# Optimization experiments

Hardware: AMD Instinct MI355X
Metric: run time of the kernel (lower is better)

## Reference

```python
import jax, jax.numpy as jnp
import numpy as np

N, E = 4096, 4096          # nodes, hyperedges
IN_DIM, OUT_DIM, EDGE_DIM = 256, 256, 64
HEADS, DEG, CARD = 8, 8, 8  # node degree, edge cardinality (regular hypergraph)


def setup_inputs() -> dict:
    key = jax.random.key(0)
    ks = jax.random.split(key, 6)
    # regular hypergraph: DEG rounds, each a permutation of nodes chunked into
    # blocks of CARD -> every node in exactly DEG edges, every edge has CARD
    # distinct nodes. E = DEG * N / CARD.
    rng = np.random.default_rng(0)
    node_of_edge = np.concatenate(
        [rng.permutation(N).reshape(-1, CARD) for _ in range(DEG)], axis=0)  # [E, CARD]
    inc = np.zeros((E, N), dtype=np.float32)
    inc[np.arange(E)[:, None], node_of_edge] = 1.0
    s = 0.05
    return {
        "x": jax.random.normal(ks[0], (N, IN_DIM), jnp.float32),
        "incidence": jnp.asarray(inc),
        "edge_attr": jax.random.normal(ks[1], (E, EDGE_DIM), jnp.float32),
        "W_lin": jax.random.normal(ks[2], (IN_DIM, OUT_DIM), jnp.float32) * s,
        "W_edge": jax.random.normal(ks[3], (EDGE_DIM, OUT_DIM), jnp.float32) * s,
        "in_proj_w": jax.random.normal(ks[4], (3 * OUT_DIM, OUT_DIM), jnp.float32) * s,
        "in_proj_b": jnp.zeros((3 * OUT_DIM,), jnp.float32),
        "out_proj_w": jax.random.normal(ks[5], (OUT_DIM, OUT_DIM), jnp.float32) * s,
        "out_proj_b": jnp.zeros((OUT_DIM,), jnp.float32),
        "deg": DEG,
        "card": CARD,
    }


def reference(x, incidence, edge_attr, W_lin, W_edge,
              in_proj_w, in_proj_b, out_proj_w, out_proj_b, deg, card):
    n = x.shape[0]
    Wh = x @ W_lin          # [N, D]
    We = edge_attr @ W_edge  # [E, D]
    Dm = Wh.shape[1]
    H = HEADS
    dh = Dm // H
    # recover regular structure from the binary incidence matrix.
    # (attention is permutation-invariant over the pair set, so the order of
    #  indices returned by top_k vs torch.nonzero does not matter)
    _, edge_of_node = jax.lax.top_k(incidence.T, deg)   # [N, deg]
    _, node_of_edge = jax.lax.top_k(incidence, card)    # [E, card]
    pair_e = edge_of_node[:, :, None]                   # [N, deg, 1]
    pair_u = node_of_edge[edge_of_node]                 # [N, deg, card]
    L = deg * card
    Ksrc = (Wh[pair_u] + We[pair_e]).reshape(n, L, Dm)  # key source per pair
    Vsrc = Wh[pair_u].reshape(n, L, Dm)                 # value source per pair
    # torch nn.MultiheadAttention in/out projections
    Wq, Wk, Wv = jnp.split(in_proj_w, 3, axis=0)
    bq, bk, bv = jnp.split(in_proj_b, 3)
    q = (Wh @ Wq.T + bq).reshape(n, H, dh)              # q_len = 1 per node
    k = (Ksrc @ Wk.T + bk).reshape(n, L, H, dh)
    v = (Vsrc @ Wv.T + bv).reshape(n, L, H, dh)
    scale = 1.0 / jnp.sqrt(jnp.asarray(dh, q.dtype))
    scores = jnp.einsum('nhd,nlhd->nhl', q, k) * scale  # [N, H, L]
    attn = jax.nn.softmax(scores, axis=-1)
    ctx = jnp.einsum('nhl,nlhd->nhd', attn, v).reshape(n, Dm)
    out = ctx @ out_proj_w.T + out_proj_b
    return jax.nn.relu(out)
```

## Files before the change

kernel.cpp:

```cpp
#include <hip/hip_runtime.h>
#include <hip/hip_bf16.h>

#define NN    4096
#define EE    4096
#define DM    256
#define EDIM  64
#define HH    8
#define DHd   32
#define LL    64

typedef short  s16x8 __attribute__((ext_vector_type(8)));
typedef unsigned short u16x8 __attribute__((ext_vector_type(8)));
typedef float  f32x4 __attribute__((ext_vector_type(4)));

__device__ __forceinline__ float b2f(unsigned short u) {
  return __uint_as_float(((unsigned int)u) << 16);
}
__device__ __forceinline__ unsigned short f2b_bits(float f) {
  unsigned int u = __float_as_uint(f);
  u = (u + 0x7FFFu + ((u >> 16) & 1u)) >> 16;
  return (unsigned short)u;
}

__global__ __launch_bounds__(256) void f2b_all(
    const float* __restrict__ x, const float* __restrict__ ea,
    const float* __restrict__ ipw, const float* __restrict__ wlin,
    const float* __restrict__ wedge, const float* __restrict__ wout,
    unsigned short* __restrict__ xb, unsigned short* __restrict__ eab,
    unsigned short* __restrict__ ipwb, unsigned short* __restrict__ wlinb,
    unsigned short* __restrict__ wedgeb, unsigned short* __restrict__ woutb,
    int* __restrict__ cnt) {
  int i = blockIdx.x * 256 + threadIdx.x;
  if (i < 8192) cnt[i] = 0;
  const float* src; unsigned short* dst; int j = i;
  if (j < 262144)       { src = x;     dst = xb; }
  else { j -= 262144;
  if (j < 65536)        { src = ea;    dst = eab; }
  else { j -= 65536;
  if (j < 49152)        { src = ipw;   dst = ipwb; }
  else { j -= 49152;
  if (j < 16384)        { src = wlin;  dst = wlinb; }
  else { j -= 16384;
  if (j < 4096)         { src = wedge; dst = wedgeb; }
  else { j -= 4096;
  if (j >= 16384) return;
                          src = wout;  dst = woutb; }}}}}
  float4 v = ((const float4*)src)[j];
  ushort4 o;
  o.x = f2b_bits(v.x); o.y = f2b_bits(v.y); o.z = f2b_bits(v.z); o.w = f2b_bits(v.w);
  ((ushort4*)dst)[j] = o;
}

#define MODE_PLAIN 0
#define MODE_PROJ  1
#define MODE_OUT   2

__device__ __forceinline__ void gemm_tile(
    const unsigned short* __restrict__ A, const unsigned short* __restrict__ B,
    int i0, int j0, int N, int K, int mode,
    float* __restrict__ out_f, unsigned short* __restrict__ out_b,
    unsigned short* __restrict__ out_b2, const float* __restrict__ bias,
    short* As, short* Bs) {
  const int tid  = threadIdx.x;
  const int wid  = tid >> 6, lane = tid & 63;
  const int wr   = (wid >> 1) * 32, wc = (wid & 1) * 32;
  const int srow = tid >> 2, schunk = (tid & 3) * 8;
  const int fr   = lane & 15, fk = (lane >> 4) * 8;

  f32x4 acc[2][2];
#pragma unroll
  for (int a = 0; a < 2; ++a)
#pragma unroll
    for (int b = 0; b < 2; ++b) acc[a][b] = (f32x4){0.f, 0.f, 0.f, 0.f};

  for (int kk = 0; kk < K; kk += 32) {
    *(s16x8*)&As[srow * 40 + schunk] = *(const s16x8*)&A[(size_t)(i0 + srow) * K + kk + schunk];
    *(s16x8*)&Bs[srow * 40 + schunk] = *(const s16x8*)&B[(size_t)(j0 + srow) * K + kk + schunk];
    __syncthreads();
    s16x8 af0 = *(const s16x8*)&As[(wr + fr) * 40 + fk];
    s16x8 af1 = *(const s16x8*)&As[(wr + 16 + fr) * 40 + fk];
    s16x8 bf0 = *(const s16x8*)&Bs[(wc + fr) * 40 + fk];
    s16x8 bf1 = *(const s16x8*)&Bs[(wc + 16 + fr) * 40 + fk];
    acc[0][0] = __builtin_amdgcn_mfma_f32_16x16x32_bf16(af0, bf0, acc[0][0], 0, 0, 0);
    acc[0][1] = __builtin_amdgcn_mfma_f32_16x16x32_bf16(af0, bf1, acc[0][1], 0, 0, 0);
    acc[1][0] = __builtin_amdgcn_mfma_f32_16x16x32_bf16(af1, bf0, acc[1][0], 0, 0, 0);
    acc[1][1] = __builtin_amdgcn_mfma_f32_16x16x32_bf16(af1, bf1, acc[1][1], 0, 0, 0);
    __syncthreads();
  }

  const int ecol = lane & 15, erow0 = (lane >> 4) * 4;
#pragma unroll
  for (int mi = 0; mi < 2; ++mi)
#pragma unroll
    for (int ni = 0; ni < 2; ++ni) {
#pragma unroll
      for (int v = 0; v < 4; ++v) {
        int i = i0 + wr + mi * 16 + erow0 + v;
        int j = j0 + wc + ni * 16 + ecol;
        float val = acc[mi][ni][v];
        if (mode == MODE_PLAIN) {
          out_b[(size_t)i * N + j] = f2b_bits(val);
        } else if (mode == MODE_PROJ) {
          if (j < 256)      out_f[(size_t)i * 256 + j]          = val + bias[j];
          else if (j < 512) out_b[(size_t)i * 256 + (j - 256)]  = f2b_bits(val);
          else              out_b2[(size_t)i * 256 + (j - 512)] = f2b_bits(val + bias[j]);
        } else {
          float r = val + bias[j];
          out_f[(size_t)i * N + j] = r > 0.f ? r : 0.f;
        }
      }
    }
}

__global__ __launch_bounds__(256) void adj_fusew(
    const float* __restrict__ inc,
    int* __restrict__ cnt_e, int* __restrict__ cnt_n,
    int* __restrict__ noe, int* __restrict__ eon,
    const unsigned short* __restrict__ ipw_bf, const unsigned short* __restrict__ wlin_bf,
    const unsigned short* __restrict__ wedg_bf,
    unsigned short* __restrict__ F, unsigned short* __restrict__ G) {
  __shared__ short As[64 * 40] __attribute__((aligned(16)));
  __shared__ short Bs[64 * 40] __attribute__((aligned(16)));
  const int bid = blockIdx.x;
  if (bid < 16384) {
    int t = bid * 256 + threadIdx.x;
    float4 v = ((const float4*)inc)[t];
    int flat = t * 4;
    int e  = flat >> 12;
    int u0 = flat & 4095;
    float vals[4] = {v.x, v.y, v.z, v.w};
#pragma unroll
    for (int j = 0; j < 4; ++j) {
      if (vals[j] != 0.0f) {
        int u  = u0 + j;
        int pe = atomicAdd(&cnt_e[e], 1);
        noe[e * 8 + pe] = u;
        int pn = atomicAdd(&cnt_n[u], 1);
        eon[u * 8 + pn] = e;
      }
    }
    return;
  }
  int fb = bid - 16384;
  if (fb < 48) {
    gemm_tile(ipw_bf, wlin_bf, (fb >> 2) * 64, (fb & 3) * 64, 256, 256,
              MODE_PLAIN, nullptr, F, nullptr, nullptr, As, Bs);
  } else {
    gemm_tile(ipw_bf + 256 * 256, wedg_bf, (fb - 48) * 64, 0, 64, 256,
              MODE_PLAIN, nullptr, G, nullptr, nullptr, As, Bs);
  }
}

__global__ __launch_bounds__(256) void proj_ke(
    const unsigned short* __restrict__ x_bf, const unsigned short* __restrict__ F,
    const unsigned short* __restrict__ ea_bf, const unsigned short* __restrict__ G,
    float* __restrict__ q, unsigned short* __restrict__ Kn, unsigned short* __restrict__ Vn,
    unsigned short* __restrict__ Ke, const float* __restrict__ ipb) {
  __shared__ short As[64 * 40] __attribute__((aligned(16)));
  __shared__ short Bs[64 * 40] __attribute__((aligned(16)));
  const int bid = blockIdx.x;
  if (bid < 768) {
    gemm_tile(x_bf, F, (bid & 63) * 64, (bid >> 6) * 64, 768, 256,
              MODE_PROJ, q, Kn, Vn, ipb, As, Bs);
  } else {
    int r = bid - 768;
    gemm_tile(ea_bf, G, (r & 63) * 64, (r >> 6) * 64, 256, 64,
              MODE_PLAIN, nullptr, Ke, nullptr, nullptr, As, Bs);
  }
}

__global__ __launch_bounds__(256) void gemm_out(
    const unsigned short* __restrict__ ctx, const unsigned short* __restrict__ wout_bf,
    float* __restrict__ out, const float* __restrict__ bias) {
  __shared__ short As[64 * 40] __attribute__((aligned(16)));
  __shared__ short Bs[64 * 40] __attribute__((aligned(16)));
  gemm_tile(ctx, wout_bf, blockIdx.x * 64, blockIdx.y * 64, 256, 256,
            MODE_OUT, out, nullptr, nullptr, bias, As, Bs);
}

__global__ __launch_bounds__(512) void attn_kernel(
    const float* __restrict__ q, const unsigned short* __restrict__ Kn,
    const unsigned short* __restrict__ Vn, const unsigned short* __restrict__ Ke,
    const int* __restrict__ eon, const int* __restrict__ noe,
    unsigned short* __restrict__ ctx) {
  const int n = blockIdx.x;
  __shared__ int   e_s[8];
  __shared__ int   u_s[64];
  __shared__ float q_s[256];
  __shared__ float qke_s[64];
  const int tid = threadIdx.x;
  if (tid < 8) e_s[tid] = eon[n * 8 + tid];
  if (tid >= 256 && tid < 320)
    ((float4*)q_s)[tid - 256] = ((const float4*)(q + (size_t)n * 256))[tid - 256];
  __syncthreads();
  if (tid < 64) {
    u_s[tid] = noe[e_s[tid >> 3] * 8 + (tid & 7)];
  } else if (tid < 128) {
    const int h = (tid - 64) >> 3, e = tid & 7;
    const u16x8* ep = (const u16x8*)(Ke + (size_t)e_s[e] * 256 + h * 32);
    float s = 0.f;
#pragma unroll
    for (int c = 0; c < 4; ++c) {
      u16x8 ev = ep[c];
#pragma unroll
      for (int j = 0; j < 8; ++j) s += q_s[h * 32 + c * 8 + j] * b2f(ev[j]);
    }
    qke_s[(h << 3) | e] = s;
  }
  __syncthreads();

  const int h = tid >> 6, lane = tid & 63;
  const int dchunk = lane >> 4, rg = lane & 15;

  u16x8 vstage[4];
#pragma unroll
  for (int i = 0; i < 4; ++i)
    vstage[i] = *(const u16x8*)(Vn + (size_t)u_s[rg * 4 + i] * 256 + h * 32 + dchunk * 8);

  const int u = u_s[lane];
  const u16x8* kp = (const u16x8*)(Kn + ((size_t)u * 256 + h * 32));
  float s = 0.f;
#pragma unroll
  for (int c = 0; c < 4; ++c) {
    u16x8 kv = kp[c];
#pragma unroll
    for (int j = 0; j < 8; ++j) s += q_s[h * 32 + c * 8 + j] * b2f(kv[j]);
  }
  s = (s + qke_s[(h << 3) | (lane >> 3)]) * 0.17677669529663687f;

  float m = s;
#pragma unroll
  for (int off = 32; off >= 1; off >>= 1) m = fmaxf(m, __shfl_xor(m, off));
  float p = __expf(s - m);
  float sum = p;
#pragma unroll
  for (int off = 32; off >= 1; off >>= 1) sum += __shfl_xor(sum, off);
  const float a = p / sum;

  float acc[8];
#pragma unroll
  for (int j = 0; j < 8; ++j) acc[j] = 0.f;
#pragma unroll
  for (int i = 0; i < 4; ++i) {
    float pi = __shfl(a, rg * 4 + i, 64);
#pragma unroll
    for (int j = 0; j < 8; ++j) acc[j] += pi * b2f(vstage[i][j]);
  }
#pragma unroll
  for (int off = 1; off < 16; off <<= 1)
#pragma unroll
    for (int j = 0; j < 8; ++j) acc[j] += __shfl_xor(acc[j], off, 64);

  if (rg == 0) {
    u16x8 o;
#pragma unroll
    for (int j = 0; j < 8; ++j) o[j] = f2b_bits(acc[j]);
    *(u16x8*)(ctx + (size_t)n * 256 + h * 32 + dchunk * 8) = o;
  }
}

#define OFF_Q      ((size_t)0)
#define OFF_KN     ((size_t)4194304)
#define OFF_VN     ((size_t)6291456)
#define OFF_KE     ((size_t)8388608)
#define OFF_CTX    ((size_t)10485760)
#define OFF_XBF    ((size_t)12582912)
#define OFF_EABF   ((size_t)14680064)
#define OFF_WOUTBF ((size_t)15204352)
#define OFF_IPWBF  ((size_t)15335424)
#define OFF_WLINBF ((size_t)15728640)
#define OFF_WEDGBF ((size_t)15859712)
#define OFF_F      ((size_t)15892480)
#define OFF_G      ((size_t)16285696)
#define OFF_CNTE   ((size_t)16318464)
#define OFF_CNTN   ((size_t)16334848)
#define OFF_NOE    ((size_t)16351232)
#define OFF_EON    ((size_t)16482304)

extern "C" void kernel_launch(void* const* d_in, const int* in_sizes, int n_in,
                              void* d_out, int out_size, void* d_ws, size_t ws_size,
                              hipStream_t stream) {
  const float* x     = (const float*)d_in[0];
  const float* inc   = (const float*)d_in[1];
  const float* ea    = (const float*)d_in[2];
  const float* wlin  = (const float*)d_in[3];
  const float* wedge = (const float*)d_in[4];
  const float* ipw   = (const float*)d_in[5];
  const float* ipb   = (const float*)d_in[6];
  const float* wout  = (const float*)d_in[7];
  const float* outb  = (const float*)d_in[8];

  char* ws = (char*)d_ws;
  float*          q       = (float*)(ws + OFF_Q);
  unsigned short* Kn      = (unsigned short*)(ws + OFF_KN);
  unsigned short* Vn      = (unsigned short*)(ws + OFF_VN);
  unsigned short* Ke      = (unsigned short*)(ws + OFF_KE);
  unsigned short* ctx     = (unsigned short*)(ws + OFF_CTX);
  unsigned short* x_bf    = (unsigned short*)(ws + OFF_XBF);
  unsigned short* ea_bf   = (unsigned short*)(ws + OFF_EABF);
  unsigned short* wout_bf = (unsigned short*)(ws + OFF_WOUTBF);
  unsigned short* ipw_bf  = (unsigned short*)(ws + OFF_IPWBF);
  unsigned short* wlin_bf = (unsigned short*)(ws + OFF_WLINBF);
  unsigned short* wedg_bf = (unsigned short*)(ws + OFF_WEDGBF);
  unsigned short* F       = (unsigned short*)(ws + OFF_F);
  unsigned short* G       = (unsigned short*)(ws + OFF_G);
  int*            cnt_e   = (int*)(ws + OFF_CNTE);
  int*            cnt_n   = (int*)(ws + OFF_CNTN);
  int*            noe     = (int*)(ws + OFF_NOE);
  int*            eon     = (int*)(ws + OFF_EON);

  f2b_all<<<1616, 256, 0, stream>>>(x, ea, ipw, wlin, wedge, wout,
                                    x_bf, ea_bf, ipw_bf, wlin_bf, wedg_bf, wout_bf,
                                    cnt_e);
  adj_fusew<<<16436, 256, 0, stream>>>(inc, cnt_e, cnt_n, noe, eon,
                                       ipw_bf, wlin_bf, wedg_bf, F, G);
  proj_ke<<<1024, 256, 0, stream>>>(x_bf, F, ea_bf, G, q, Kn, Vn, Ke, ipb);
  attn_kernel<<<4096, 512, 0, stream>>>(q, Kn, Vn, Ke, eon, noe, ctx);
  gemm_out<<<dim3(64, 4), 256, 0, stream>>>(ctx, wout_bf, (float*)d_out, outb);
}
```

Measured before the change: 83.51 us.

## Fuse conversion into adjacency kernel, precompute pair indices, restructure attention per wave

The separate fp32-to-bf16 conversion kernel is removed. Activation conversion is merged into the adjacency-building kernel, weight-product GEMMs now read fp32 weights directly, and the counter zeroing moves to a memset. Q is stored as bf16 with the softmax scale folded into the projection epilogue. Pair node indices are precomputed in the projection kernel, and attention now runs one wave per (node, head) with no shared memory or block syncs. The aim is fewer launches, less traffic and less synchronisation, at the cost of extra bf16 rounding of q and a memset launch.

```diff
diff --git a/kernel.cpp b/kernel.cpp
--- a/kernel.cpp
+++ b/kernel.cpp
@@ -13,6 +13,8 @@
 typedef unsigned short u16x8 __attribute__((ext_vector_type(8)));
 typedef float  f32x4 __attribute__((ext_vector_type(4)));
 
+#define SCALE 0.17677669529663687f
+
 __device__ __forceinline__ float b2f(unsigned short u) {
   return __uint_as_float(((unsigned int)u) << 16);
 }
@@ -22,38 +24,21 @@
   return (unsigned short)u;
 }
 
-__global__ __launch_bounds__(256) void f2b_all(
-    const float* __restrict__ x, const float* __restrict__ ea,
-    const float* __restrict__ ipw, const float* __restrict__ wlin,
-    const float* __restrict__ wedge, const float* __restrict__ wout,
-    unsigned short* __restrict__ xb, unsigned short* __restrict__ eab,
-    unsigned short* __restrict__ ipwb, unsigned short* __restrict__ wlinb,
-    unsigned short* __restrict__ wedgeb, unsigned short* __restrict__ woutb,
-    int* __restrict__ cnt) {
-  int i = blockIdx.x * 256 + threadIdx.x;
-  if (i < 8192) cnt[i] = 0;
-  const float* src; unsigned short* dst; int j = i;
-  if (j < 262144)       { src = x;     dst = xb; }
-  else { j -= 262144;
-  if (j < 65536)        { src = ea;    dst = eab; }
-  else { j -= 65536;
-  if (j < 49152)        { src = ipw;   dst = ipwb; }
-  else { j -= 49152;
-  if (j < 16384)        { src = wlin;  dst = wlinb; }
-  else { j -= 16384;
-  if (j < 4096)         { src = wedge; dst = wedgeb; }
-  else { j -= 4096;
-  if (j >= 16384) return;
-                          src = wout;  dst = woutb; }}}}}
-  float4 v = ((const float4*)src)[j];
-  ushort4 o;
-  o.x = f2b_bits(v.x); o.y = f2b_bits(v.y); o.z = f2b_bits(v.z); o.w = f2b_bits(v.w);
-  ((ushort4*)dst)[j] = o;
-}
-
 #define MODE_PLAIN 0
 #define MODE_PROJ  1
 #define MODE_OUT   2
+
+__device__ __forceinline__ void gemm_mfma_body(
+    short* As, short* Bs, f32x4 acc[2][2], int wr, int wc, int fr, int fk) {
+  s16x8 af0 = *(const s16x8*)&As[(wr + fr) * 40 + fk];
+  s16x8 af1 = *(const s16x8*)&As[(wr + 16 + fr) * 40 + fk];
+  s16x8 bf0 = *(const s16x8*)&Bs[(wc + fr) * 40 + fk];
+  s16x8 bf1 = *(const s16x8*)&Bs[(wc + 16 + fr) * 40 + fk];
+  acc[0][0] = __builtin_amdgcn_mfma_f32_16x16x32_bf16(af0, bf0, acc[0][0], 0, 0, 0);
+  acc[0][1] = __builtin_amdgcn_mfma_f32_16x16x32_bf16(af0, bf1, acc[0][1], 0, 0, 0);
+  acc[1][0] = __builtin_amdgcn_mfma_f32_16x16x32_bf16(af1, bf0, acc[1][0], 0, 0, 0);
+  acc[1][1] = __builtin_amdgcn_mfma_f32_16x16x32_bf16(af1, bf1, acc[1][1], 0, 0, 0);
+}
 
 __device__ __forceinline__ void gemm_tile(
     const unsigned short* __restrict__ A, const unsigned short* __restrict__ B,
@@ -77,14 +62,7 @@
     *(s16x8*)&As[srow * 40 + schunk] = *(const s16x8*)&A[(size_t)(i0 + srow) * K + kk + schunk];
     *(s16x8*)&Bs[srow * 40 + schunk] = *(const s16x8*)&B[(size_t)(j0 + srow) * K + kk + schunk];
     __syncthreads();
-    s16x8 af0 = *(const s16x8*)&As[(wr + fr) * 40 + fk];
-    s16x8 af1 = *(const s16x8*)&As[(wr + 16 + fr) * 40 + fk];
-    s16x8 bf0 = *(const s16x8*)&Bs[(wc + fr) * 40 + fk];
-    s16x8 bf1 = *(const s16x8*)&Bs[(wc + 16 + fr) * 40 + fk];
-    acc[0][0] = __builtin_amdgcn_mfma_f32_16x16x32_bf16(af0, bf0, acc[0][0], 0, 0, 0);
-    acc[0][1] = __builtin_amdgcn_mfma_f32_16x16x32_bf16(af0, bf1, acc[0][1], 0, 0, 0);
-    acc[1][0] = __builtin_amdgcn_mfma_f32_16x16x32_bf16(af1, bf0, acc[1][0], 0, 0, 0);
-    acc[1][1] = __builtin_amdgcn_mfma_f32_16x16x32_bf16(af1, bf1, acc[1][1], 0, 0, 0);
+    gemm_mfma_body(As, Bs, acc, wr, wc, fr, fk);
     __syncthreads();
   }
 
@@ -101,9 +79,9 @@
         if (mode == MODE_PLAIN) {
           out_b[(size_t)i * N + j] = f2b_bits(val);
         } else if (mode == MODE_PROJ) {
-          if (j < 256)      out_f[(size_t)i * 256 + j]          = val + bias[j];
-          else if (j < 512) out_b[(size_t)i * 256 + (j - 256)]  = f2b_bits(val);
-          else              out_b2[(size_t)i * 256 + (j - 512)] = f2b_bits(val + bias[j]);
+          if (j < 256)      out_b[(size_t)i * 256 + j]           = f2b_bits((val + bias[j]) * SCALE);
+          else if (j < 512) out_b2[(size_t)i * 256 + (j - 256)]  = f2b_bits(val);
+          else              ((unsigned short*)out_f)[(size_t)i * 256 + (j - 512)] = f2b_bits(val + bias[j]);
         } else {
           float r = val + bias[j];
           out_f[(size_t)i * N + j] = r > 0.f ? r : 0.f;
@@ -112,12 +90,66 @@
     }
 }
 
-__global__ __launch_bounds__(256) void adj_fusew(
+__device__ __forceinline__ void gemm_tile_f32src(
+    const float* __restrict__ A, const float* __restrict__ B,
+    int i0, int j0, int N, int K,
+    unsigned short* __restrict__ out_b, short* As, short* Bs) {
+  const int tid  = threadIdx.x;
+  const int wid  = tid >> 6, lane = tid & 63;
+  const int wr   = (wid >> 1) * 32, wc = (wid & 1) * 32;
+  const int srow = tid >> 2, schunk = (tid & 3) * 8;
+  const int fr   = lane & 15, fk = (lane >> 4) * 8;
+
+  f32x4 acc[2][2];
+#pragma unroll
+  for (int a = 0; a < 2; ++a)
+#pragma unroll
+    for (int b = 0; b < 2; ++b) acc[a][b] = (f32x4){0.f, 0.f, 0.f, 0.f};
+
+  for (int kk = 0; kk < K; kk += 32) {
+    float4 a0 = *(const float4*)&A[(size_t)(i0 + srow) * K + kk + schunk];
+    float4 a1 = *(const float4*)&A[(size_t)(i0 + srow) * K + kk + schunk + 4];
+    float4 b0 = *(const float4*)&B[(size_t)(j0 + srow) * K + kk + schunk];
+    float4 b1 = *(const float4*)&B[(size_t)(j0 + srow) * K + kk + schunk + 4];
+    s16x8 av, bv;
+    av[0] = (short)f2b_bits(a0.x); av[1] = (short)f2b_bits(a0.y);
+    av[2] = (short)f2b_bits(a0.z); av[3] = (short)f2b_bits(a0.w);
+    av[4] = (short)f2b_bits(a1.x); av[5] = (short)f2b_bits(a1.y);
+    av[6] = (short)f2b_bits(a1.z); av[7] = (short)f2b_bits(a1.w);
+    bv[0] = (short)f2b_bits(b0.x); bv[1] = (short)f2b_bits(b0.y);
+    bv[2] = (short)f2b_bits(b0.z); bv[3] = (short)f2b_bits(b0.w);
+    bv[4] = (short)f2b_bits(b1.x); bv[5] = (short)f2b_bits(b1.y);
+    bv[6] = (short)f2b_bits(b1.z); bv[7] = (short)f2b_bits(b1.w);
+    *(s16x8*)&As[srow * 40 + schunk] = av;
+    *(s16x8*)&Bs[srow * 40 + schunk] = bv;
+    __syncthreads();
+    gemm_mfma_body(As, Bs, acc, wr, wc, fr, fk);
+    __syncthreads();
+  }
+
+  const int ecol = lane & 15, erow0 = (lane >> 4) * 4;
+#pragma unroll
+  for (int mi = 0; mi < 2; ++mi)
+#pragma unroll
+    for (int ni = 0; ni < 2; ++ni)
+#pragma unroll
+      for (int v = 0; v < 4; ++v) {
+        int i = i0 + wr + mi * 16 + erow0 + v;
+        int j = j0 + wc + ni * 16 + ecol;
+        if (j < N) out_b[(size_t)i * N + j] = f2b_bits(acc[mi][ni][v]);
+      }
+}
+
+__global__ __launch_bounds__(256) void mega1(
     const float* __restrict__ inc,
     int* __restrict__ cnt_e, int* __restrict__ cnt_n,
     int* __restrict__ noe, int* __restrict__ eon,
-    const unsigned short* __restrict__ ipw_bf, const unsigned short* __restrict__ wlin_bf,
-    const unsigned short* __restrict__ wedg_bf,
+    const float* __restrict__ x, const float* __restrict__ ea,
+    const float* __restrict__ wout,
+    unsigned short* __restrict__ xb, unsigned short* __restrict__ eab,
+    unsigned short* __restrict__ woutb,
+    const float* __restrict__ ipw, const float* __restrict__ wlin,
+    const float* __restrict__ wedge,
     unsigned short* __restrict__ F, unsigned short* __restrict__ G) {
   __shared__ short As[64 * 40] __attribute__((aligned(16)));
   __shared__ short Bs[64 * 40] __attribute__((aligned(16)));
@@ -141,31 +173,118 @@
     }
     return;
   }
-  int fb = bid - 16384;
+  if (bid < 17728) {
+    int j = (bid - 16384) * 256 + threadIdx.x;
+    const float* src; unsigned short* dst;
+    if (j < 262144)      { src = x;    dst = xb; }
+    else { j -= 262144;
+    if (j < 65536)       { src = ea;   dst = eab; }
+    else { j -= 65536;     src = wout; dst = woutb; } }
+    float4 v = ((const float4*)src)[j];
+    ushort4 o;
+    o.x = f2b_bits(v.x); o.y = f2b_bits(v.y); o.z = f2b_bits(v.z); o.w = f2b_bits(v.w);
+    ((ushort4*)dst)[j] = o;
+    return;
+  }
+  int fb = bid - 17728;
   if (fb < 48) {
-    gemm_tile(ipw_bf, wlin_bf, (fb >> 2) * 64, (fb & 3) * 64, 256, 256,
-              MODE_PLAIN, nullptr, F, nullptr, nullptr, As, Bs);
+    gemm_tile_f32src(ipw, wlin, (fb >> 2) * 64, (fb & 3) * 64, 256, 256, F, As, Bs);
   } else {
-    gemm_tile(ipw_bf + 256 * 256, wedg_bf, (fb - 48) * 64, 0, 64, 256,
-              MODE_PLAIN, nullptr, G, nullptr, nullptr, As, Bs);
-  }
-}
-
-__global__ __launch_bounds__(256) void proj_ke(
+    gemm_tile_f32src(ipw + 65536, wedge, (fb - 48) * 64, 0, 64, 256, G, As, Bs);
+  }
+}
+
+__global__ __launch_bounds__(256) void mega2(
     const unsigned short* __restrict__ x_bf, const unsigned short* __restrict__ F,
     const unsigned short* __restrict__ ea_bf, const unsigned short* __restrict__ G,
-    float* __restrict__ q, unsigned short* __restrict__ Kn, unsigned short* __restrict__ Vn,
-    unsigned short* __restrict__ Ke, const float* __restrict__ ipb) {
+    unsigned short* __restrict__ Q, unsigned short* __restrict__ Kn,
+    unsigned short* __restrict__ Vn, unsigned short* __restrict__ Ke,
+    const float* __restrict__ ipb,
+    const int* __restrict__ eon, const int* __restrict__ noe,
+    int* __restrict__ pair_u) {
   __shared__ short As[64 * 40] __attribute__((aligned(16)));
   __shared__ short Bs[64 * 40] __attribute__((aligned(16)));
   const int bid = blockIdx.x;
   if (bid < 768) {
     gemm_tile(x_bf, F, (bid & 63) * 64, (bid >> 6) * 64, 768, 256,
-              MODE_PROJ, q, Kn, Vn, ipb, As, Bs);
-  } else {
+              MODE_PROJ, (float*)Vn, Q, Kn, ipb, As, Bs);
+  } else if (bid < 1024) {
     int r = bid - 768;
     gemm_tile(ea_bf, G, (r & 63) * 64, (r >> 6) * 64, 256, 64,
               MODE_PLAIN, nullptr, Ke, nullptr, nullptr, As, Bs);
+  } else {
+    int wv = ((bid - 1024) * 256 + threadIdx.x) >> 6;
+    int lane = threadIdx.x & 63;
+#pragma unroll
+    for (int r = 0; r < 16; ++r) {
+      int n = wv * 16 + r;
+      int e = eon[n * 8 + (lane >> 3)];
+      pair_u[n * 64 + lane] = noe[e * 8 + (lane & 7)];
+    }
+  }
+}
+
+__global__ __launch_bounds__(256) void attn_kernel(
+    const unsigned short* __restrict__ Q, const unsigned short* __restrict__ Kn,
+    const unsigned short* __restrict__ Vn, const unsigned short* __restrict__ Ke,
+    const int* __restrict__ eon, const int* __restrict__ pair_u,
+    unsigned short* __restrict__ ctx) {
+  const int w = (blockIdx.x * 256 + threadIdx.x) >> 6;
+  const int n = w >> 3, h = w & 7;
+  const int lane = threadIdx.x & 63;
+  const int rg = lane & 15, dchunk = lane >> 4;
+
+  const int u = pair_u[n * 64 + lane];
+  const int e = eon[n * 8 + (lane >> 3)];
+
+  int ur[4];
+#pragma unroll
+  for (int i = 0; i < 4; ++i) ur[i] = __shfl(u, rg * 4 + i, 64);
+  u16x8 vstage[4];
+#pragma unroll
+  for (int i = 0; i < 4; ++i)
+    vstage[i] = *(const u16x8*)(Vn + (size_t)ur[i] * 256 + h * 32 + dchunk * 8);
+
+  const u16x8* kp = (const u16x8*)(Kn + (size_t)u * 256 + h * 32);
+  const u16x8* ep = (const u16x8*)(Ke + (size_t)e * 256 + h * 32);
+  const u16x8* qp = (const u16x8*)(Q  + (size_t)n * 256 + h * 32);
+  float s = 0.f;
+#pragma unroll
+  for (int c = 0; c < 4; ++c) {
+    u16x8 kv = kp[c], ev = ep[c], qv = qp[c];
+#pragma unroll
+    for (int j = 0; j < 8; ++j)
+      s += b2f(qv[j]) * (b2f(kv[j]) + b2f(ev[j]));
+  }
+
+  float m = s;
+#pragma unroll
+  for (int off = 32; off >= 1; off >>= 1) m = fmaxf(m, __shfl_xor(m, off));
+  float p = __expf(s - m);
+  float sum = p;
+#pragma unroll
+  for (int off = 32; off >= 1; off >>= 1) sum += __shfl_xor(sum, off);
+  const float a = __fdividef(p, sum);
+
+  float acc[8];
+#pragma unroll
+  for (int j = 0; j < 8; ++j) acc[j] = 0.f;
+#pragma unroll
+  for (int i = 0; i < 4; ++i) {
+    float pi = __shfl(a, rg * 4 + i, 64);
+#pragma unroll
+    for (int j = 0; j < 8; ++j) acc[j] += pi * b2f(vstage[i][j]);
+  }
+#pragma unroll
+  for (int off = 1; off < 16; off <<= 1)
+#pragma unroll
+    for (int j = 0; j < 8; ++j) acc[j] += __shfl_xor(acc[j], off, 64);
+
+  if (rg == 0) {
+    u16x8 o;
+#pragma unroll
+    for (int j = 0; j < 8; ++j) o[j] = f2b_bits(acc[j]);
+    *(u16x8*)(ctx + (size_t)n * 256 + h * 32 + dchunk * 8) = o;
   }
 }
 
@@ -178,104 +297,22 @@
             MODE_OUT, out, nullptr, nullptr, bias, As, Bs);
 }
 
-__global__ __launch_bounds__(512) void attn_kernel(
-    const float* __restrict__ q, const unsigned short* __restrict__ Kn,
-    const unsigned short* __restrict__ Vn, const unsigned short* __restrict__ Ke,
-    const int* __restrict__ eon, const int* __restrict__ noe,
-    unsigned short* __restrict__ ctx) {
-  const int n = blockIdx.x;
-  __shared__ int   e_s[8];
-  __shared__ int   u_s[64];
-  __shared__ float q_s[256];
-  __shared__ float qke_s[64];
-  const int tid = threadIdx.x;
-  if (tid < 8) e_s[tid] = eon[n * 8 + tid];
-  if (tid >= 256 && tid < 320)
-    ((float4*)q_s)[tid - 256] = ((const float4*)(q + (size_t)n * 256))[tid - 256];
-  __syncthreads();
-  if (tid < 64) {
-    u_s[tid] = noe[e_s[tid >> 3] * 8 + (tid & 7)];
-  } else if (tid < 128) {
-    const int h = (tid - 64) >> 3, e = tid & 7;
-    const u16x8* ep = (const u16x8*)(Ke + (size_t)e_s[e] * 256 + h * 32);
-    float s = 0.f;
-#pragma unroll
-    for (int c = 0; c < 4; ++c) {
-      u16x8 ev = ep[c];
-#pragma unroll
-      for (int j = 0; j < 8; ++j) s += q_s[h * 32 + c * 8 + j] * b2f(ev[j]);
-    }
-    qke_s[(h << 3) | e] = s;
-  }
-  __syncthreads();
-
-  const int h = tid >> 6, lane = tid & 63;
-  const int dchunk = lane >> 4, rg = lane & 15;
-
-  u16x8 vstage[4];
-#pragma unroll
-  for (int i = 0; i < 4; ++i)
-    vstage[i] = *(const u16x8*)(Vn + (size_t)u_s[rg * 4 + i] * 256 + h * 32 + dchunk * 8);
-
-  const int u = u_s[lane];
-  const u16x8* kp = (const u16x8*)(Kn + ((size_t)u * 256 + h * 32));
-  float s = 0.f;
-#pragma unroll
-  for (int c = 0; c < 4; ++c) {
-    u16x8 kv = kp[c];
-#pragma unroll
-    for (int j = 0; j < 8; ++j) s += q_s[h * 32 + c * 8 + j] * b2f(kv[j]);
-  }
-  s = (s + qke_s[(h << 3) | (lane >> 3)]) * 0.17677669529663687f;
-
-  float m = s;
-#pragma unroll
-  for (int off = 32; off >= 1; off >>= 1) m = fmaxf(m, __shfl_xor(m, off));
-  float p = __expf(s - m);
-  float sum = p;
-#pragma unroll
-  for (int off = 32; off >= 1; off >>= 1) sum += __shfl_xor(sum, off);
-  const float a = p / sum;
-
-  float acc[8];
-#pragma unroll
-  for (int j = 0; j < 8; ++j) acc[j] = 0.f;
-#pragma unroll
-  for (int i = 0; i < 4; ++i) {
-    float pi = __shfl(a, rg * 4 + i, 64);
-#pragma unroll
-    for (int j = 0; j < 8; ++j) acc[j] += pi * b2f(vstage[i][j]);
-  }
-#pragma unroll
-  for (int off = 1; off < 16; off <<= 1)
-#pragma unroll
-    for (int j = 0; j < 8; ++j) acc[j] += __shfl_xor(acc[j], off, 64);
-
-  if (rg == 0) {
-    u16x8 o;
-#pragma unroll
-    for (int j = 0; j < 8; ++j) o[j] = f2b_bits(acc[j]);
-    *(u16x8*)(ctx + (size_t)n * 256 + h * 32 + dchunk * 8) = o;
-  }
-}
-
+#define MB_ ((size_t)1048576)
 #define OFF_Q      ((size_t)0)
-#define OFF_KN     ((size_t)4194304)
-#define OFF_VN     ((size_t)6291456)
-#define OFF_KE     ((size_t)8388608)
-#define OFF_CTX    ((size_t)10485760)
-#define OFF_XBF    ((size_t)12582912)
-#define OFF_EABF   ((size_t)14680064)
-#define OFF_WOUTBF ((size_t)15204352)
-#define OFF_IPWBF  ((size_t)15335424)
-#define OFF_WLINBF ((size_t)15728640)
-#define OFF_WEDGBF ((size_t)15859712)
-#define OFF_F      ((size_t)15892480)
-#define OFF_G      ((size_t)16285696)
-#define OFF_CNTE   ((size_t)16318464)
-#define OFF_CNTN   ((size_t)16334848)
-#define OFF_NOE    ((size_t)16351232)
-#define OFF_EON    ((size_t)16482304)
+#define OFF_KN     (2*MB_)
+#define OFF_VN     (4*MB_)
+#define OFF_KE     (6*MB_)
+#define OFF_CTX    (8*MB_)
+#define OFF_XBF    (10*MB_)
+#define OFF_EABF   (12*MB_)
+#define OFF_WOUTBF (12*MB_+524288)
+#define OFF_F      (13*MB_)
+#define OFF_G      (13*MB_+524288)
+#define OFF_PAIRU  (14*MB_)
+#define OFF_CNTE   (15*MB_)
+#define OFF_CNTN   (15*MB_+16384)
+#define OFF_NOE    (15*MB_+32768)
+#define OFF_EON    (15*MB_+163840)
 
 extern "C" void kernel_launch(void* const* d_in, const int* in_sizes, int n_in,
                               void* d_out, int out_size, void* d_ws, size_t ws_size,
@@ -291,7 +328,7 @@
   const float* outb  = (const float*)d_in[8];
 
   char* ws = (char*)d_ws;
-  float*          q       = (float*)(ws + OFF_Q);
+  unsigned short* Q       = (unsigned short*)(ws + OFF_Q);
   unsigned short* Kn      = (unsigned short*)(ws + OFF_KN);
   unsigned short* Vn      = (unsigned short*)(ws + OFF_VN);
   unsigned short* Ke      = (unsigned short*)(ws + OFF_KE);
@@ -299,22 +336,20 @@
   unsigned short* x_bf    = (unsigned short*)(ws + OFF_XBF);
   unsigned short* ea_bf   = (unsigned short*)(ws + OFF_EABF);
   unsigned short* wout_bf = (unsigned short*)(ws + OFF_WOUTBF);
-  unsigned short* ipw_bf  = (unsigned short*)(ws + OFF_IPWBF);
-  unsigned short* wlin_bf = (unsigned short*)(ws + OFF_WLINBF);
-  unsigned short* wedg_bf = (unsigned short*)(ws + OFF_WEDGBF);
   unsigned short* F       = (unsigned short*)(ws + OFF_F);
   unsigned short* G       = (unsigned short*)(ws + OFF_G);
   int*            cnt_e   = (int*)(ws + OFF_CNTE);
-  int*            cnt_n   = (int*)(ws + OFF_CNTN);
   int*            noe     = (int*)(ws + OFF_NOE);
   int*            eon     = (int*)(ws + OFF_EON);
-
-  f2b_all<<<1616, 256, 0, stream>>>(x, ea, ipw, wlin, wedge, wout,
-                                    x_bf, ea_bf, ipw_bf, wlin_bf, wedg_bf, wout_bf,
-                                    cnt_e);
-  adj_fusew<<<16436, 256, 0, stream>>>(inc, cnt_e, cnt_n, noe, eon,
-                                       ipw_bf, wlin_bf, wedg_bf, F, G);
-  proj_ke<<<1024, 256, 0, stream>>>(x_bf, F, ea_bf, G, q, Kn, Vn, Ke, ipb);
-  attn_kernel<<<4096, 512, 0, stream>>>(q, Kn, Vn, Ke, eon, noe, ctx);
+  int*            pair_u  = (int*)(ws + OFF_PAIRU);
+
+  hipMemsetAsync(ws + OFF_CNTE, 0, 32768, stream);
+
+  mega1<<<17780, 256, 0, stream>>>(inc, cnt_e, (int*)(ws + OFF_CNTN), noe, eon,
+                                   x, ea, wout, x_bf, ea_bf, wout_bf,
+                                   ipw, wlin, wedge, F, G);
+  mega2<<<1088, 256, 0, stream>>>(x_bf, F, ea_bf, G, Q, Kn, Vn, Ke, ipb,
+                                  eon, noe, pair_u);
+  attn_kernel<<<8192, 256, 0, stream>>>(Q, Kn, Vn, Ke, eon, pair_u, ctx);
   gemm_out<<<dim3(64, 4), 256, 0, stream>>>(ctx, wout_bf, (float*)d_out, outb);
 }
```

Result: slower. 92.20 us (+10.4%).
